# Kernel tuning notes

Measured on AMD Instinct MI355X. Metric: run time of the kernel, lower is better.

## Reference

```python
import jax, jax.numpy as jnp
import numpy as np

ALPHA = 0.5        # self._alpha
MAX_COEFF = 10.0   # self._max_coeff
SHARPNESS = 5      # self._loss_sharpness

N_VARS = 1_000_000
N_CLAUSES = 4_000_000
N_EDGES = 12_000_000


def setup_inputs() -> dict:
    key = jax.random.key(0)
    k1, k2, k3, k4 = jax.random.split(key, 4)
    variable_prediction = jax.random.uniform(k1, (N_VARS, 1), dtype=jnp.float32)
    lits = jax.random.randint(k2, (N_EDGES,), 0, N_VARS, dtype=jnp.int32)
    clauses = jax.random.randint(k3, (N_EDGES,), 0, N_CLAUSES, dtype=jnp.int32)
    graph_map = jnp.stack([lits, clauses])  # [2, E]
    # literal polarity: +1 (positive literal) or -1 (negated literal)
    edge_feature = jnp.where(jax.random.bernoulli(k4, 0.5, (N_EDGES, 1)), 1.0, -1.0).astype(jnp.float32)
    return {
        "variable_prediction": variable_prediction,
        "graph_map": graph_map,
        "edge_feature": edge_feature,
        "num_clauses": N_CLAUSES,
        "global_step": jnp.array([100.0], dtype=jnp.float32),
        "eps": jnp.array([1e-10], dtype=jnp.float32),
    }


def reference(variable_prediction, graph_map, edge_feature, num_clauses, global_step, eps):
    # temperature coefficient: min(step^alpha, max_coeff)
    coeff = jnp.minimum(global_step ** ALPHA, MAX_COEFF)  # [1]
    lits = graph_map[0]     # [E] variable index per edge
    clauses = graph_map[1]  # [E] clause index per edge
    ef = edge_feature[:, 0]  # [E]

    # sparse mm (signed variable mask @ prediction) == signed gather
    edge_values = ef * variable_prediction[lits, 0]          # [E]
    edge_values = edge_values + (1.0 - ef) * 0.5             # negated literal -> 1 - p
    weights = jnp.exp(coeff * edge_values)                   # [E]

    # sparse mm (function mask @ .) == scatter-add over clauses
    nominator = jax.ops.segment_sum(weights * edge_values, clauses, num_segments=num_clauses)
    denominator = jax.ops.segment_sum(weights, clauses, num_segments=num_clauses)

    clause_value = denominator / jnp.maximum(nominator, eps)
    clause_value = 1.0 + (clause_value - 1.0) ** SHARPNESS
    return jnp.mean(jnp.log(jnp.maximum(clause_value, eps)))
```

## Files before the change

kernel.cpp:

```cpp
#include <hip/hip_runtime.h>
#include <math.h>


constexpr int   N_CLAUSES_C = 4000000;
constexpr int   BKT_SHIFT   = 12;
constexpr int   BKT_CLS     = 1 << BKT_SHIFT;
constexpr int   NB_TOTAL    = (N_CLAUSES_C + BKT_CLS - 1) >> BKT_SHIFT;
constexpr int   CAP         = 13056;
constexpr int   SC_THREADS  = 1024;
constexpr int   BATCH       = 8192;
constexpr int   SC_CHUNK    = 3 * BATCH;
constexpr int   PR_THREADS  = 512;

__device__ __forceinline__ uint32_t ev_enc(float ev) {
    return (__float_as_uint(ev) + 0x400u) >> 11;
}
__device__ __forceinline__ float ev_dec(uint32_t q) {
    return __uint_as_float(q << 11);
}

__global__ __launch_bounds__(SC_THREADS) void
scatter_kernel(const float* __restrict__ vp,
               const int* __restrict__ lits,
               const int* __restrict__ cls,
               const float* __restrict__ ef,
               uint32_t* __restrict__ payload,
               uint32_t* __restrict__ cursors,
               int n_edges, int b_lo, int b_hi) {
    __shared__ uint32_t bh[NB_TOTAL];
    __shared__ uint32_t bOff[NB_TOTAL];
    __shared__ uint32_t bb[NB_TOTAL];
    __shared__ uint32_t buf[BATCH];
    __shared__ uint16_t bufB[BATCH];
    __shared__ uint32_t wsums[16];
    __shared__ uint32_t totalS;

    const int tid  = threadIdx.x;
    const int lane = tid & 63;
    const int wv   = tid >> 6;
    const int nbp  = b_hi - b_lo;
    const int c0   = blockIdx.x * SC_CHUNK;
    const int c1   = min(n_edges, c0 + SC_CHUNK);

    for (int batch = 0; batch < (SC_CHUNK / BATCH); ++batch) {
        const int ebase = c0 + batch * BATCH;
        if (ebase >= c1) break;
        if (tid < nbp) bh[tid] = 0;
        __syncthreads();

        uint32_t ent[8]; uint16_t ebk[8]; uint16_t ern[8];
        #pragma unroll
        for (int i = 0; i < 8; ++i) {
            ebk[i] = 0xFFFFu;
            int e = ebase + i * SC_THREADS + tid;
            if (e < c1) {
                int c = __builtin_nontemporal_load(cls + e);
                int b = c >> BKT_SHIFT;
                if (b >= b_lo && b < b_hi) {
                    int   l = __builtin_nontemporal_load(lits + e);
                    float f = __builtin_nontemporal_load(ef + e);
                    float ev = fmaf(f, vp[l], (1.0f - f) * 0.5f);
                    ev = fminf(fmaxf(ev, 0.0f), 1.0f);
                    uint32_t evq = ev_enc(ev);
                    int ib = b - b_lo;
                    uint32_t r = atomicAdd(&bh[ib], 1u);
                    ent[i] = (evq << BKT_SHIFT) | (uint32_t)(c & (BKT_CLS - 1));
                    ebk[i] = (uint16_t)ib;
                    ern[i] = (uint16_t)r;
                }
            }
        }
        __syncthreads();

        uint32_t v = (tid < nbp) ? bh[tid] : 0u;
        uint32_t x = v;
        #pragma unroll
        for (int d = 1; d < 64; d <<= 1) {
            uint32_t n = __shfl_up(x, (unsigned)d, 64);
            if (lane >= d) x += n;
        }
        if (lane == 63) wsums[wv] = x;
        __syncthreads();
        if (wv == 0) {
            uint32_t s = (lane < 16) ? wsums[lane] : 0u;
            uint32_t y = s;
            #pragma unroll
            for (int d = 1; d < 16; d <<= 1) {
                uint32_t n = __shfl_up(y, (unsigned)d, 64);
                if (lane >= d) y += n;
            }
            if (lane < 16) wsums[lane] = y - s;
        }
        __syncthreads();
        uint32_t incl = x + wsums[wv];
        if (tid < nbp) {
            bOff[tid] = incl - v;
            bb[tid]   = v ? atomicAdd(&cursors[b_lo + tid], v) : 0u;
        }
        if (tid == SC_THREADS - 1) totalS = incl;
        __syncthreads();

        #pragma unroll
        for (int i = 0; i < 8; ++i) {
            if (ebk[i] != 0xFFFFu) {
                uint32_t s = bOff[ebk[i]] + ern[i];
                buf[s]  = ent[i];
                bufB[s] = ebk[i];
            }
        }
        __syncthreads();

        const uint32_t tS = totalS;
        for (uint32_t s = tid; s < tS; s += SC_THREADS) {
            uint32_t ib   = bufB[s];
            uint32_t gpos = bb[ib] + (s - bOff[ib]);
            if (gpos < (uint32_t)CAP)
                payload[(size_t)ib * CAP + gpos] = buf[s];
        }
        __syncthreads();
    }
}

__global__ __launch_bounds__(PR_THREADS) void
process_kernel(const uint32_t* __restrict__ payload,
               const uint32_t* __restrict__ cursors,
               const float* __restrict__ gstep,
               const float* __restrict__ epsp,
               double* __restrict__ acc,
               int b_lo) {
    __shared__ uint32_t offp[BKT_CLS / 2];
    __shared__ uint32_t srt[CAP];
    __shared__ uint32_t wscan[8];
    __shared__ double   wsum[8];
    const int tid  = threadIdx.x;
    const int lane = tid & 63;
    const int wv   = tid >> 6;
    const int b    = b_lo + blockIdx.x;

    for (int j = tid; j < BKT_CLS / 2; j += PR_THREADS) offp[j] = 0;
    __syncthreads();

    const uint32_t cnt = min(cursors[b], (uint32_t)CAP);
    const uint32_t* pl = payload + (size_t)blockIdx.x * CAP;
    const uint32_t nv = cnt >> 2;

    for (uint32_t k = tid; k < nv; k += PR_THREADS) {
        uint4 p4 = ((const uint4*)pl)[k];
        uint32_t c;
        c = p4.x & (BKT_CLS - 1); atomicAdd(&offp[c >> 1], 1u << ((c & 1) << 4));
        c = p4.y & (BKT_CLS - 1); atomicAdd(&offp[c >> 1], 1u << ((c & 1) << 4));
        c = p4.z & (BKT_CLS - 1); atomicAdd(&offp[c >> 1], 1u << ((c & 1) << 4));
        c = p4.w & (BKT_CLS - 1); atomicAdd(&offp[c >> 1], 1u << ((c & 1) << 4));
    }
    for (uint32_t k = (nv << 2) + tid; k < cnt; k += PR_THREADS) {
        uint32_t c = pl[k] & (BKT_CLS - 1);
        atomicAdd(&offp[c >> 1], 1u << ((c & 1) << 4));
    }
    __syncthreads();

    uint32_t pk[4];
    const int jb = tid * 4;
    uint32_t t = 0;
    #pragma unroll
    for (int i = 0; i < 4; ++i) {
        pk[i] = offp[jb + i];
        t += (pk[i] & 0xFFFFu) + (pk[i] >> 16);
    }
    uint32_t x = t;
    #pragma unroll
    for (int d = 1; d < 64; d <<= 1) {
        uint32_t n = __shfl_up(x, (unsigned)d, 64);
        if (lane >= d) x += n;
    }
    if (lane == 63) wscan[wv] = x;
    __syncthreads();
    if (tid == 0) {
        uint32_t r = 0;
        #pragma unroll
        for (int w = 0; w < 8; ++w) { uint32_t tm = wscan[w]; wscan[w] = r; r += tm; }
    }
    __syncthreads();
    uint32_t run = (x - t) + wscan[wv];
    #pragma unroll
    for (int i = 0; i < 4; ++i) {
        uint32_t lo = pk[i] & 0xFFFFu, hi = pk[i] >> 16;
        offp[jb + i] = run | ((run + lo) << 16);
        run += lo + hi;
    }
    __syncthreads();

    for (uint32_t k = tid; k < nv; k += PR_THREADS) {
        uint4 p4 = ((const uint4*)pl)[k];
        #pragma unroll
        for (int j = 0; j < 4; ++j) {
            uint32_t p = (j == 0) ? p4.x : (j == 1) ? p4.y : (j == 2) ? p4.z : p4.w;
            uint32_t c = p & (BKT_CLS - 1);
            uint32_t sh = (c & 1) << 4;
            uint32_t r = atomicAdd(&offp[c >> 1], 1u << sh);
            srt[(r >> sh) & 0xFFFFu] = p;
        }
    }
    for (uint32_t k = (nv << 2) + tid; k < cnt; k += PR_THREADS) {
        uint32_t p = pl[k];
        uint32_t c = p & (BKT_CLS - 1);
        uint32_t sh = (c & 1) << 4;
        uint32_t r = atomicAdd(&offp[c >> 1], 1u << sh);
        srt[(r >> sh) & 0xFFFFu] = p;
    }
    __syncthreads();

    const float coeff = fminf(sqrtf(gstep[0]), 10.0f);
    const float eps   = epsp[0];
    const int gbase = b << BKT_SHIFT;
    double local = 0.0;
    for (int j = tid; j < BKT_CLS; j += PR_THREADS) {
        if (gbase + j < N_CLAUSES_C) {
            uint32_t e = (offp[j >> 1] >> ((j & 1) << 4)) & 0xFFFFu;
            uint32_t s = 0;
            if (j > 0) {
                int jm = j - 1;
                s = (offp[jm >> 1] >> ((jm & 1) << 4)) & 0xFFFFu;
            }
            float nom = 0.f, den = 0.f;
            for (uint32_t k = s; k < e; ++k) {
                float ev = ev_dec(srt[k] >> BKT_SHIFT);
                float w  = __expf(coeff * ev);
                nom = fmaf(w, ev, nom);
                den += w;
            }
            float cv = den / fmaxf(nom, eps);
            float tt = cv - 1.0f;
            float t2 = tt * tt;
            float cv2 = 1.0f + t2 * t2 * tt;
            local += (double)__logf(fmaxf(cv2, eps));
        }
    }
    #pragma unroll
    for (int off = 32; off > 0; off >>= 1) local += __shfl_down(local, off, 64);
    if (lane == 0) wsum[wv] = local;
    __syncthreads();
    if (tid == 0) {
        double s = 0.0;
        #pragma unroll
        for (int w = 0; w < 8; ++w) s += wsum[w];
        unsafeAtomicAdd(acc, s);
    }
}

__global__ void finalize_kernel(const double* __restrict__ acc,
                                const int* __restrict__ ncp,
                                float* __restrict__ out) {
    if (threadIdx.x == 0 && blockIdx.x == 0)
        out[0] = (float)(acc[0] / (double)ncp[0]);
}

extern "C" void kernel_launch(void* const* d_in, const int* in_sizes, int n_in,
                              void* d_out, int out_size, void* d_ws, size_t ws_size,
                              hipStream_t stream) {
    const float* vp    = (const float*)d_in[0];
    const int*   gmap  = (const int*)d_in[1];
    const float* ef    = (const float*)d_in[2];
    const int*   ncp   = (const int*)d_in[3];
    const float* gstep = (const float*)d_in[4];
    const float* epsp  = (const float*)d_in[5];
    float*       out   = (float*)d_out;

    const int n_edges = in_sizes[1] / 2;
    const int* lits = gmap;
    const int* cls  = gmap + n_edges;

    int P = 8;
    int nbp_max = (NB_TOTAL + 7) / 8;
    size_t cursors_off_w = (size_t)nbp_max * CAP;
    size_t acc_off_w = (cursors_off_w + NB_TOTAL + 1) & ~(size_t)1;
    const int cands[4] = {1, 2, 4, 8};
    for (int ci = 0; ci < 4; ++ci) {
        int cand = cands[ci];
        int nm = (NB_TOTAL + cand - 1) / cand;
        size_t pw = (size_t)nm * CAP;
        size_t cw = pw + NB_TOTAL;
        size_t aw = (cw + 1) & ~(size_t)1;
        size_t need = aw * 4 + 8;
        if (need <= ws_size) { P = cand; nbp_max = nm; cursors_off_w = pw; acc_off_w = aw; break; }
    }

    uint32_t* payload = (uint32_t*)d_ws;
    uint32_t* cursors = payload + cursors_off_w;
    double*   acc     = (double*)((uint32_t*)d_ws + acc_off_w);

    hipMemsetAsync(cursors, 0, (acc_off_w - cursors_off_w) * 4 + 8, stream);

    const int sc_blocks = (n_edges + SC_CHUNK - 1) / SC_CHUNK;
    for (int p = 0; p < P; ++p) {
        int b_lo = p * nbp_max;
        int b_hi = min(NB_TOTAL, b_lo + nbp_max);
        if (b_lo >= b_hi) continue;
        scatter_kernel<<<sc_blocks, SC_THREADS, 0, stream>>>(
            vp, lits, cls, ef, payload, cursors, n_edges, b_lo, b_hi);
        process_kernel<<<b_hi - b_lo, PR_THREADS, 0, stream>>>(
            payload, cursors, gstep, epsp, acc, b_lo);
    }
    finalize_kernel<<<1, 64, 0, stream>>>(acc, ncp, out);
}
```

Measured before the change: 181.2 us.

## Vectorize scatter loads, halve block size, and batch gathers ahead of atomics

The scatter kernel now runs 512 threads per block with 4096-edge batches. Each thread loads 8 contiguous edges with 128-bit nontemporal vector loads, and all 8 vp gathers are issued before the shared-memory atomics so memory latency can overlap. Edge polarity is tested via the sign bit of the float reinterpreted as int, and the final clamp is removed. Each thread handles two buckets in the scan, and the cross-wave prefix is done serially by one thread. This raises occupancy and load efficiency, but the contiguous per-thread edge assignment changes the order in which edges are appended within a bucket.

```diff
diff --git a/kernel.cpp b/kernel.cpp
--- a/kernel.cpp
+++ b/kernel.cpp
@@ -7,10 +7,13 @@
 constexpr int   BKT_CLS     = 1 << BKT_SHIFT;
 constexpr int   NB_TOTAL    = (N_CLAUSES_C + BKT_CLS - 1) >> BKT_SHIFT;
 constexpr int   CAP         = 13056;
-constexpr int   SC_THREADS  = 1024;
-constexpr int   BATCH       = 8192;
-constexpr int   SC_CHUNK    = 3 * BATCH;
+constexpr int   SC_THREADS  = 512;
+constexpr int   BATCH       = 4096;
+constexpr int   NBATCH      = 3;
+constexpr int   SC_CHUNK    = BATCH * NBATCH;
 constexpr int   PR_THREADS  = 512;
+
+typedef int v4i __attribute__((ext_vector_type(4)));
 
 __device__ __forceinline__ uint32_t ev_enc(float ev) {
     return (__float_as_uint(ev) + 0x400u) >> 11;
@@ -19,11 +22,11 @@
     return __uint_as_float(q << 11);
 }
 
-__global__ __launch_bounds__(SC_THREADS) void
+__global__ __launch_bounds__(SC_THREADS, 8) void
 scatter_kernel(const float* __restrict__ vp,
                const int* __restrict__ lits,
                const int* __restrict__ cls,
-               const float* __restrict__ ef,
+               const int* __restrict__ efi,
                uint32_t* __restrict__ payload,
                uint32_t* __restrict__ cursors,
                int n_edges, int b_lo, int b_hi) {
@@ -32,7 +35,7 @@
     __shared__ uint32_t bb[NB_TOTAL];
     __shared__ uint32_t buf[BATCH];
     __shared__ uint16_t bufB[BATCH];
-    __shared__ uint32_t wsums[16];
+    __shared__ uint32_t wsums[8];
     __shared__ uint32_t totalS;
 
     const int tid  = threadIdx.x;
@@ -41,39 +44,68 @@
     const int nbp  = b_hi - b_lo;
     const int c0   = blockIdx.x * SC_CHUNK;
     const int c1   = min(n_edges, c0 + SC_CHUNK);
-
-    for (int batch = 0; batch < (SC_CHUNK / BATCH); ++batch) {
+    const int j0   = 2 * tid, j1 = 2 * tid + 1;
+
+    for (int batch = 0; batch < NBATCH; ++batch) {
         const int ebase = c0 + batch * BATCH;
         if (ebase >= c1) break;
-        if (tid < nbp) bh[tid] = 0;
-        __syncthreads();
-
-        uint32_t ent[8]; uint16_t ebk[8]; uint16_t ern[8];
+        for (int i = tid; i < nbp; i += SC_THREADS) bh[i] = 0;
+        __syncthreads();
+
+        const int base = ebase + tid * 8;
+        int cc[8], ll[8], ss[8];
+        if (base + 8 <= c1) {
+            v4i ca = __builtin_nontemporal_load((const v4i*)(cls  + base));
+            v4i cb = __builtin_nontemporal_load((const v4i*)(cls  + base + 4));
+            v4i la = __builtin_nontemporal_load((const v4i*)(lits + base));
+            v4i lb = __builtin_nontemporal_load((const v4i*)(lits + base + 4));
+            v4i fa = __builtin_nontemporal_load((const v4i*)(efi  + base));
+            v4i fb = __builtin_nontemporal_load((const v4i*)(efi  + base + 4));
+            #pragma unroll
+            for (int i = 0; i < 4; ++i) {
+                cc[i] = ca[i]; cc[4 + i] = cb[i];
+                ll[i] = la[i]; ll[4 + i] = lb[i];
+                ss[i] = fa[i]; ss[4 + i] = fb[i];
+            }
+        } else {
+            #pragma unroll
+            for (int i = 0; i < 8; ++i) {
+                int e = base + i;
+                if (e < c1) { cc[i] = cls[e]; ll[i] = lits[e]; ss[i] = efi[e]; }
+                else cc[i] = -1;
+            }
+        }
+
+        float vv[8];
+        #pragma unroll
+        for (int i = 0; i < 8; ++i) vv[i] = (cc[i] >= 0) ? vp[ll[i]] : 0.0f;
+
+        uint16_t ebk[8], ern[8];
         #pragma unroll
         for (int i = 0; i < 8; ++i) {
             ebk[i] = 0xFFFFu;
-            int e = ebase + i * SC_THREADS + tid;
-            if (e < c1) {
-                int c = __builtin_nontemporal_load(cls + e);
-                int b = c >> BKT_SHIFT;
+            if (cc[i] >= 0) {
+                int b = cc[i] >> BKT_SHIFT;
                 if (b >= b_lo && b < b_hi) {
-                    int   l = __builtin_nontemporal_load(lits + e);
-                    float f = __builtin_nontemporal_load(ef + e);
-                    float ev = fmaf(f, vp[l], (1.0f - f) * 0.5f);
-                    ev = fminf(fmaxf(ev, 0.0f), 1.0f);
-                    uint32_t evq = ev_enc(ev);
                     int ib = b - b_lo;
-                    uint32_t r = atomicAdd(&bh[ib], 1u);
-                    ent[i] = (evq << BKT_SHIFT) | (uint32_t)(c & (BKT_CLS - 1));
                     ebk[i] = (uint16_t)ib;
-                    ern[i] = (uint16_t)r;
+                    ern[i] = (uint16_t)atomicAdd(&bh[ib], 1u);
                 }
             }
         }
-        __syncthreads();
-
-        uint32_t v = (tid < nbp) ? bh[tid] : 0u;
-        uint32_t x = v;
+        uint32_t ent[8];
+        #pragma unroll
+        for (int i = 0; i < 8; ++i) {
+            if (ebk[i] != 0xFFFFu) {
+                float ev = (ss[i] >= 0) ? vv[i] : (1.0f - vv[i]);
+                ent[i] = (ev_enc(ev) << BKT_SHIFT) | (uint32_t)(cc[i] & (BKT_CLS - 1));
+            }
+        }
+        __syncthreads();
+
+        uint32_t v0 = (j0 < nbp) ? bh[j0] : 0u;
+        uint32_t v1 = (j1 < nbp) ? bh[j1] : 0u;
+        uint32_t t = v0 + v1, x = t;
         #pragma unroll
         for (int d = 1; d < 64; d <<= 1) {
             uint32_t n = __shfl_up(x, (unsigned)d, 64);
@@ -81,23 +113,16 @@
         }
         if (lane == 63) wsums[wv] = x;
         __syncthreads();
-        if (wv == 0) {
-            uint32_t s = (lane < 16) ? wsums[lane] : 0u;
-            uint32_t y = s;
+        if (tid == 0) {
+            uint32_t r = 0;
             #pragma unroll
-            for (int d = 1; d < 16; d <<= 1) {
-                uint32_t n = __shfl_up(y, (unsigned)d, 64);
-                if (lane >= d) y += n;
-            }
-            if (lane < 16) wsums[lane] = y - s;
-        }
-        __syncthreads();
-        uint32_t incl = x + wsums[wv];
-        if (tid < nbp) {
-            bOff[tid] = incl - v;
-            bb[tid]   = v ? atomicAdd(&cursors[b_lo + tid], v) : 0u;
-        }
-        if (tid == SC_THREADS - 1) totalS = incl;
+            for (int w = 0; w < 8; ++w) { uint32_t tm = wsums[w]; wsums[w] = r; r += tm; }
+        }
+        __syncthreads();
+        uint32_t run = (x - t) + wsums[wv];
+        if (j0 < nbp) { bOff[j0] = run;      bb[j0] = v0 ? atomicAdd(&cursors[b_lo + j0], v0) : 0u; }
+        if (j1 < nbp) { bOff[j1] = run + v0; bb[j1] = v1 ? atomicAdd(&cursors[b_lo + j1], v1) : 0u; }
+        if (tid == SC_THREADS - 1) totalS = x + wsums[wv];
         __syncthreads();
 
         #pragma unroll
@@ -296,7 +321,7 @@
         int b_hi = min(NB_TOTAL, b_lo + nbp_max);
         if (b_lo >= b_hi) continue;
         scatter_kernel<<<sc_blocks, SC_THREADS, 0, stream>>>(
-            vp, lits, cls, ef, payload, cursors, n_edges, b_lo, b_hi);
+            vp, lits, cls, (const int*)ef, payload, cursors, n_edges, b_lo, b_hi);
         process_kernel<<<b_hi - b_lo, PR_THREADS, 0, stream>>>(
             payload, cursors, gstep, epsp, acc, b_lo);
     }
```

After: 234.3 us. 1.29x slower.
